# Performance work log

Measured on AMD Instinct MI355X. Metric: run time of the kernel, lower is better.

The kernel has to match this reference:

```python
import jax, jax.numpy as jnp
import numpy as np
import math

D = 256      # d_model
HEADS = 8
PTS = 4      # num_points
L = 6        # num_layers
FF = 1024    # dim_feedforward
B = 8
HS, WS = 100, 100  # feature map -> N = 10000
HD = D // HEADS


def setup_inputs() -> dict:
    key = jax.random.key(0)
    ks = jax.random.split(key, 8)
    w = lambda k, shape, s: jax.random.normal(k, shape, jnp.float32) * s
    z = lambda *shape: jnp.zeros(shape, jnp.float32)
    return {
        "src": jax.random.normal(ks[0], (B, HS * WS, D), jnp.float32),
        "Wv": w(ks[1], (L, D, D), 0.02), "bv": z(L, D),
        "Woff": w(ks[2], (L, D, HEADS * PTS * 2), 0.01), "boff": z(L, HEADS * PTS * 2),
        "Wa": w(ks[3], (L, D, HEADS * PTS), 0.02), "ba": z(L, HEADS * PTS),
        "Wo": w(ks[4], (L, D, D), 0.02), "bo": z(L, D),
        "W1": w(ks[5], (L, D, FF), 0.02), "b1": z(L, FF),
        "W2": w(ks[6], (L, FF, D), 0.02), "b2": z(L, D),
        "g1": jnp.ones((L, D)), "be1": z(L, D),
        "g2": jnp.ones((L, D)), "be2": z(L, D),
        "H": HS, "W": WS,
    }


def pos_encoding_2d(d_model, H, W):
    # standard 2D sine encoding: first half of channels encode y, second half x
    half = d_model // 2
    freqs = jnp.exp(-math.log(10000.0) * jnp.arange(0, half, 2, dtype=jnp.float32) / half)
    ya = jnp.arange(H, dtype=jnp.float32)[:, None] * freqs[None, :]
    xa = jnp.arange(W, dtype=jnp.float32)[:, None] * freqs[None, :]
    pe_y = jnp.stack([jnp.sin(ya), jnp.cos(ya)], -1).reshape(H, half)
    pe_x = jnp.stack([jnp.sin(xa), jnp.cos(xa)], -1).reshape(W, half)
    pe = jnp.concatenate([
        jnp.broadcast_to(pe_y[:, None, :], (H, W, half)),
        jnp.broadcast_to(pe_x[None, :, :], (H, W, half))], -1)
    return pe.reshape(H * W, d_model)


def layer_norm(x, g, b, eps=1e-5):
    m = x.mean(-1, keepdims=True)
    v = ((x - m) ** 2).mean(-1, keepdims=True)
    return (x - m) * jax.lax.rsqrt(v + eps) * g + b


def deform_attn(q, Wv, bv, Woff, boff, Wa, ba, Wo, bo, H, W):
    # single-scale Deformable-DETR attention; q: [B, N, D], N = H*W
    Bq, N, _ = q.shape
    v = (q @ Wv + bv).reshape(Bq, N, HEADS, HD)
    off = (q @ Woff + boff).reshape(Bq, N, HEADS, PTS, 2)          # (dx, dy) in pixels
    attn = jax.nn.softmax((q @ Wa + ba).reshape(Bq, N, HEADS, PTS), axis=-1)
    # reference points: normalized grid cell centers
    ys, xs = jnp.meshgrid(jnp.arange(H, dtype=jnp.float32),
                          jnp.arange(W, dtype=jnp.float32), indexing='ij')
    ref = jnp.stack([(xs.reshape(-1) + 0.5) / W, (ys.reshape(-1) + 0.5) / H], -1)  # [N,2]
    loc = ref[None, :, None, None, :] + off / jnp.array([W, H], jnp.float32)       # [B,N,h,P,2]
    # pixel coords, align_corners=False; border padding via clamping
    px = loc[..., 0] * W - 0.5
    py = loc[..., 1] * H - 0.5
    x0 = jnp.floor(px); y0 = jnp.floor(py)
    wx = px - x0; wy = py - y0
    x0i = jnp.clip(x0.astype(jnp.int32), 0, W - 1); x1i = jnp.clip(x0i + 1, 0, W - 1)
    y0i = jnp.clip(y0.astype(jnp.int32), 0, H - 1); y1i = jnp.clip(y0i + 1, 0, H - 1)
    vbh = v.transpose(0, 2, 1, 3).reshape(Bq * HEADS, N, HD)       # [B*h, N, hd]
    flat = lambda yi, xi: (yi * W + xi).transpose(0, 2, 1, 3).reshape(Bq * HEADS, N * PTS)
    gather = jax.vmap(lambda val, idx: val[idx])                   # [B*h, N*P, hd]
    wxr = wx.transpose(0, 2, 1, 3).reshape(Bq * HEADS, N * PTS, 1)
    wyr = wy.transpose(0, 2, 1, 3).reshape(Bq * HEADS, N * PTS, 1)
    s = (gather(vbh, flat(y0i, x0i)) * (1 - wxr) * (1 - wyr)
         + gather(vbh, flat(y0i, x1i)) * wxr * (1 - wyr)
         + gather(vbh, flat(y1i, x0i)) * (1 - wxr) * wyr
         + gather(vbh, flat(y1i, x1i)) * wxr * wyr)
    s = s.reshape(Bq, HEADS, N, PTS, HD)
    out = jnp.einsum('bhnp,bhnpd->bhnd', attn.transpose(0, 2, 1, 3), s)
    out = out.transpose(0, 2, 1, 3).reshape(Bq, N, D)
    return out @ Wo + bo


def reference(src, Wv, bv, Woff, boff, Wa, ba, Wo, bo, W1, b1, W2, b2,
              g1, be1, g2, be2, H, W):
    x = src + pos_encoding_2d(D, H, W)[None]
    for i in range(L):
        a = deform_attn(x, Wv[i], bv[i], Woff[i], boff[i], Wa[i], ba[i], Wo[i], bo[i], H, W)
        x = layer_norm(x + a, g1[i], be1[i])
        h = jax.nn.gelu(x @ W1[i] + b1[i], approximate=False)
        x = layer_norm(x + (h @ W2[i] + b2[i]), g2[i], be2[i])
    return x
```

## Files before the change

### kernel.cpp

```cpp
#include <hip/hip_runtime.h>
#include <hip/hip_bf16.h>
#include <math.h>

#define Bq   8
#define NPix 10000
#define HH   100
#define WW   100
#define Dm   256
#define NH   8
#define HD   32
#define PTS  4
#define FFd  1024
#define Lnum 6
#define Mrows (Bq * NPix)

typedef short bf16x8 __attribute__((ext_vector_type(8)));
typedef float f32x4 __attribute__((ext_vector_type(4)));

__device__ __forceinline__ float bf2f(unsigned short u) {
    return __uint_as_float(((unsigned)u) << 16);
}
__device__ __forceinline__ unsigned short f2bf(float f) {
    unsigned x = __float_as_uint(f);
    return (unsigned short)((x + 0x7fffu + ((x >> 16) & 1u)) >> 16);
}
__device__ __forceinline__ float gelu_t(float v) {
    float z = 1.5957691216f * (v + 0.044715f * v * v * v);
    float e = __expf(z);
    float th = 1.0f - 2.0f / (e + 1.0f);
    return 0.5f * v * (1.0f + th);
}

__global__ __launch_bounds__(256) void pos_add_kernel(
    const float* __restrict__ src, float* __restrict__ x, short* __restrict__ xb)
{
    int idx = blockIdx.x * 256 + threadIdx.x;
    int c = idx & (Dm - 1);
    int n = (idx >> 8) % NPix;
    int cc = c;
    float coord;
    if (c < 128) { coord = (float)(n / WW); }
    else         { coord = (float)(n % WW); cc = c - 128; }
    int j = cc >> 1;
    float f = __expf(-logf(10000.0f) * (2.0f * (float)j) / 128.0f);
    float arg = coord * f;
    float pe = (cc & 1) ? cosf(arg) : sinf(arg);
    float val = src[idx] + pe;
    x[idx] = val;
    xb[idx] = (short)f2bf(val);
}

__global__ __launch_bounds__(256) void repack_kernel(
    const float* __restrict__ W, short* __restrict__ Wt,
    int K, int N, int outLstride, int nOff)
{
    __shared__ float t[64][65];
    int l  = blockIdx.z;
    int k0 = blockIdx.y * 64, n0 = blockIdx.x * 64;
    const float* Wl = W + (size_t)l * K * N;
    for (int i = threadIdx.x; i < 64 * 64; i += 256) {
        int kk = i >> 6, nn = i & 63;
        float val = 0.0f;
        if (k0 + kk < K && n0 + nn < N) val = Wl[(size_t)(k0 + kk) * N + (n0 + nn)];
        t[kk][nn] = val;
    }
    __syncthreads();
    for (int i = threadIdx.x; i < 64 * 64; i += 256) {
        int nn = i >> 6, kk = i & 63;
        if (n0 + nn < N && k0 + kk < K)
            Wt[(size_t)l * outLstride + (size_t)(nOff + n0 + nn) * K + (k0 + kk)]
                = (short)f2bf(t[kk][nn]);
    }
}

__global__ void bcat_kernel(const float* __restrict__ bv,
                            const float* __restrict__ boff,
                            const float* __restrict__ ba,
                            float* __restrict__ bcat)
{
    int l = blockIdx.x, c = threadIdx.x;
    float v;
    if (c < 256)      v = bv[l * 256 + c];
    else if (c < 320) v = boff[l * 64 + (c - 256)];
    else              v = ba[l * 32 + (c - 320)];
    bcat[l * 352 + c] = v;
}

template<int KI, int MODE>
__global__ __launch_bounds__(256) void gemm_mfma_kernel(
    const short* __restrict__ A, const short* __restrict__ Bt,
    const float* __restrict__ bias, short* __restrict__ Cv,
    float* __restrict__ C2,
    int M, int Nc, int ldc)
{
    constexpr int K = KI * 64;
    __shared__ short As[128 * 64];
    __shared__ short Bs[128 * 64];
    const int tid = threadIdx.x;

    int nwg  = gridDim.x * gridDim.y;
    int orig = blockIdx.y * gridDim.x + blockIdx.x;
    int xcd  = orig & 7, pos = orig >> 3;
    int q = nwg >> 3, r = nwg & 7;
    int flat = (xcd < r ? xcd * (q + 1) : r * (q + 1) + (xcd - r) * q) + pos;
    const int bm = (flat / gridDim.x) * 128;
    const int bn = (flat % gridDim.x) * 128;

    const int w = tid >> 6, l = tid & 63;
    const int wr = (w >> 1) * 64, wc = (w & 1) * 64;
    const int rl = tid >> 3;
    const int cl = tid & 7;
    const int lr = l & 15, lq = l >> 4;

    const short* pA[4]; const short* pB[4];
    #pragma unroll
    for (int p = 0; p < 4; ++p) {
        int row = p * 32 + rl;
        int sc  = cl ^ (row & 7);
        int ga  = bm + row; if (ga > M - 1) ga = M - 1;
        pA[p] = A + (size_t)ga * K + sc * 8;
        int gb  = bn + row; if (gb > Nc - 1) gb = Nc - 1;
        pB[p] = Bt + (size_t)gb * K + sc * 8;
    }

    int aoff[2][4], boff[2][4];
    #pragma unroll
    for (int ks = 0; ks < 2; ++ks)
        #pragma unroll
        for (int m = 0; m < 4; ++m) {
            int ra = wr + m * 16 + lr;
            aoff[ks][m] = ra * 64 + (((ks * 4 + lq) ^ (ra & 7))) * 8;
            int rb = wc + m * 16 + lr;
            boff[ks][m] = rb * 64 + (((ks * 4 + lq) ^ (rb & 7))) * 8;
        }

    f32x4 acc[4][4];
    #pragma unroll
    for (int m = 0; m < 4; ++m)
        #pragma unroll
        for (int n = 0; n < 4; ++n)
            #pragma unroll
            for (int j = 0; j < 4; ++j) acc[m][n][j] = 0.0f;

    #pragma unroll
    for (int kc = 0; kc < KI; ++kc) {
        #pragma unroll
        for (int p = 0; p < 4; ++p) {
            __builtin_amdgcn_global_load_lds((const void*)pA[p],
                (void*)&As[(p * 32 + w * 8) * 64], 16, 0, 0);
            pA[p] += 64;
            __builtin_amdgcn_global_load_lds((const void*)pB[p],
                (void*)&Bs[(p * 32 + w * 8) * 64], 16, 0, 0);
            pB[p] += 64;
        }
        __syncthreads();

        #pragma unroll
        for (int ks = 0; ks < 2; ++ks) {
            bf16x8 af[4], bfr[4];
            #pragma unroll
            for (int m = 0; m < 4; ++m) af[m]  = *(const bf16x8*)&As[aoff[ks][m]];
            #pragma unroll
            for (int n = 0; n < 4; ++n) bfr[n] = *(const bf16x8*)&Bs[boff[ks][n]];
            #pragma unroll
            for (int m = 0; m < 4; ++m)
                #pragma unroll
                for (int n = 0; n < 4; ++n)
                    acc[m][n] = __builtin_amdgcn_mfma_f32_16x16x32_bf16(
                        af[m], bfr[n], acc[m][n], 0, 0, 0);
        }
        __syncthreads();
    }

    #pragma unroll
    for (int m = 0; m < 4; ++m) {
        int row0 = bm + wr + m * 16 + lq * 4;
        #pragma unroll
        for (int n = 0; n < 4; ++n) {
            int col = bn + wc + n * 16 + lr;
            if (MODE == 2 && col >= Nc) continue;
            float bi = bias[col];
            #pragma unroll
            for (int j = 0; j < 4; ++j) {
                int rr = row0 + j;
                if (rr >= M) continue;
                float val = acc[m][n][j] + bi;
                if (MODE == 0) {
                    Cv[(size_t)rr * ldc + col] = (short)f2bf(gelu_t(val));
                } else {
                    if (col < 256)
                        Cv[(size_t)rr * 256 + col] = (short)f2bf(val);
                    else
                        C2[(size_t)rr * 96 + (col - 256)] = val;
                }
            }
        }
    }
}

template<int KI>
__global__ __launch_bounds__(256) void gemm_ln_kernel(
    const short* __restrict__ A, const short* __restrict__ Bt,
    const float* __restrict__ bias,
    const float* __restrict__ gw, const float* __restrict__ bw,
    float* __restrict__ x, short* __restrict__ xb,
    int M)
{
    constexpr int K = KI * 64;
    __shared__ short As[64 * 64];
    __shared__ short Bs[256 * 64];
    const int tid = threadIdx.x;
    const int bm = blockIdx.x * 64;
    const int w = tid >> 6, l = tid & 63;
    const int rl = tid >> 3, cl = tid & 7;
    const int lr = l & 15, lq = l >> 4;

    const short* pA[2]; const short* pB[8];
    #pragma unroll
    for (int p = 0; p < 2; ++p) {
        int row = p * 32 + rl;
        int sc  = cl ^ (row & 7);
        int ga  = bm + row; if (ga > M - 1) ga = M - 1;
        pA[p] = A + (size_t)ga * K + sc * 8;
    }
    #pragma unroll
    for (int p = 0; p < 8; ++p) {
        int row = p * 32 + rl;
        int sc  = cl ^ (row & 7);
        pB[p] = Bt + (size_t)row * K + sc * 8;
    }

    const int arow = w * 16 + lr;
    int aoff[2];
    #pragma unroll
    for (int ks = 0; ks < 2; ++ks)
        aoff[ks] = arow * 64 + (((ks * 4 + lq) ^ (arow & 7))) * 8;
    int boff[2][16];
    #pragma unroll
    for (int ks = 0; ks < 2; ++ks)
        #pragma unroll
        for (int i = 0; i < 16; ++i) {
            int brow = i * 16 + lr;
            boff[ks][i] = brow * 64 + (((ks * 4 + lq) ^ (brow & 7))) * 8;
        }

    f32x4 acc[16];
    #pragma unroll
    for (int n = 0; n < 16; ++n)
        #pragma unroll
        for (int j = 0; j < 4; ++j) acc[n][j] = 0.0f;

    #pragma unroll
    for (int kc = 0; kc < KI; ++kc) {
        #pragma unroll
        for (int p = 0; p < 2; ++p) {
            __builtin_amdgcn_global_load_lds((const void*)pA[p],
                (void*)&As[(p * 32 + w * 8) * 64], 16, 0, 0);
            pA[p] += 64;
        }
        #pragma unroll
        for (int p = 0; p < 8; ++p) {
            __builtin_amdgcn_global_load_lds((const void*)pB[p],
                (void*)&Bs[(p * 32 + w * 8) * 64], 16, 0, 0);
            pB[p] += 64;
        }
        __syncthreads();

        #pragma unroll
        for (int ks = 0; ks < 2; ++ks) {
            bf16x8 af = *(const bf16x8*)&As[aoff[ks]];
            #pragma unroll
            for (int hb = 0; hb < 2; ++hb) {
                bf16x8 bfr[8];
                #pragma unroll
                for (int i = 0; i < 8; ++i)
                    bfr[i] = *(const bf16x8*)&Bs[boff[ks][hb * 8 + i]];
                #pragma unroll
                for (int i = 0; i < 8; ++i)
                    acc[hb * 8 + i] = __builtin_amdgcn_mfma_f32_16x16x32_bf16(
                        af, bfr[i], acc[hb * 8 + i], 0, 0, 0);
            }
        }
        __syncthreads();
    }

    float bi[16];
    #pragma unroll
    for (int n = 0; n < 16; ++n) bi[n] = bias[n * 16 + lr];

    #pragma unroll
    for (int j = 0; j < 4; ++j) {
        int rr = bm + w * 16 + lq * 4 + j;
        if (rr < M) {
            float tmp[16];
            float sum = 0.0f;
            #pragma unroll
            for (int n = 0; n < 16; ++n) {
                int c = n * 16 + lr;
                float val = acc[n][j] + bi[n] + x[(size_t)rr * 256 + c];
                tmp[n] = val;
                sum += val;
            }
            #pragma unroll
            for (int o = 8; o >= 1; o >>= 1) sum += __shfl_xor(sum, o);
            float mean = sum * (1.0f / 256.0f);
            float vs = 0.0f;
            #pragma unroll
            for (int n = 0; n < 16; ++n) {
                float d = tmp[n] - mean;
                vs += d * d;
            }
            #pragma unroll
            for (int o = 8; o >= 1; o >>= 1) vs += __shfl_xor(vs, o);
            float rstd = rsqrtf(vs * (1.0f / 256.0f) + 1e-5f);
            #pragma unroll
            for (int n = 0; n < 16; ++n) {
                int c = n * 16 + lr;
                float ov = (tmp[n] - mean) * rstd * gw[c] + bw[c];
                x[(size_t)rr * 256 + c] = ov;
                xb[(size_t)rr * 256 + c] = (short)f2bf(ov);
            }
        }
    }
}

__global__ __launch_bounds__(256) void deform_attn_kernel(
    const short* __restrict__ v, const float* __restrict__ comb,
    short* __restrict__ outs)
{
    int g  = blockIdx.x * 16 + (threadIdx.x >> 4);
    int d2 = threadIdx.x & 15;
    int bn = g >> 3, h = g & 7;
    int n  = bn % NPix;
    int row = n / WW, col = n % WW;
    int base_v = (bn / NPix) * NPix;

    const float* cb = comb + (size_t)bn * 96;
    float l0 = cb[64 + h * 4 + 0], l1 = cb[64 + h * 4 + 1];
    float l2 = cb[64 + h * 4 + 2], l3 = cb[64 + h * 4 + 3];
    float mx = fmaxf(fmaxf(l0, l1), fmaxf(l2, l3));
    float e0 = __expf(l0 - mx), e1 = __expf(l1 - mx);
    float e2 = __expf(l2 - mx), e3 = __expf(l3 - mx);
    float inv = 1.0f / (e0 + e1 + e2 + e3);
    float aw[4] = {e0 * inv, e1 * inv, e2 * inv, e3 * inv};

    float acc0 = 0.0f, acc1 = 0.0f;
    size_t chb = (size_t)h * HD + d2 * 2;
    #pragma unroll
    for (int p = 0; p < 4; ++p) {
        float dx = cb[h * 8 + p * 2 + 0];
        float dy = cb[h * 8 + p * 2 + 1];
        float px = (float)col + dx;
        float py = (float)row + dy;
        float x0f = floorf(px), y0f = floorf(py);
        float wx = px - x0f, wy = py - y0f;
        int x0i = min(max((int)x0f, 0), WW - 1);
        int y0i = min(max((int)y0f, 0), HH - 1);
        int x1i = min(x0i + 1, WW - 1);
        int y1i = min(y0i + 1, HH - 1);
        unsigned u00 = *(const unsigned*)&v[(size_t)(base_v + y0i * WW + x0i) * Dm + chb];
        unsigned u01 = *(const unsigned*)&v[(size_t)(base_v + y0i * WW + x1i) * Dm + chb];
        unsigned u10 = *(const unsigned*)&v[(size_t)(base_v + y1i * WW + x0i) * Dm + chb];
        unsigned u11 = *(const unsigned*)&v[(size_t)(base_v + y1i * WW + x1i) * Dm + chb];
        float w00 = (1.0f - wx) * (1.0f - wy), w01 = wx * (1.0f - wy);
        float w10 = (1.0f - wx) * wy,          w11 = wx * wy;
        float s0 = bf2f((unsigned short)u00) * w00 + bf2f((unsigned short)u01) * w01
                 + bf2f((unsigned short)u10) * w10 + bf2f((unsigned short)u11) * w11;
        float s1 = bf2f((unsigned short)(u00 >> 16)) * w00 + bf2f((unsigned short)(u01 >> 16)) * w01
                 + bf2f((unsigned short)(u10 >> 16)) * w10 + bf2f((unsigned short)(u11 >> 16)) * w11;
        acc0 = fmaf(aw[p], s0, acc0);
        acc1 = fmaf(aw[p], s1, acc1);
    }
    unsigned outw = (unsigned)f2bf(acc0) | ((unsigned)f2bf(acc1) << 16);
    *(unsigned*)&outs[(size_t)bn * Dm + chb] = outw;
}

extern "C" void kernel_launch(void* const* d_in, const int* in_sizes, int n_in,
                              void* d_out, int out_size, void* d_ws, size_t ws_size,
                              hipStream_t stream)
{
    const float* src  = (const float*)d_in[0];
    const float* Wv   = (const float*)d_in[1];
    const float* bv   = (const float*)d_in[2];
    const float* Woff = (const float*)d_in[3];
    const float* boff = (const float*)d_in[4];
    const float* Wa   = (const float*)d_in[5];
    const float* ba   = (const float*)d_in[6];
    const float* Wo   = (const float*)d_in[7];
    const float* bo   = (const float*)d_in[8];
    const float* W1   = (const float*)d_in[9];
    const float* b1   = (const float*)d_in[10];
    const float* W2   = (const float*)d_in[11];
    const float* b2   = (const float*)d_in[12];
    const float* g1   = (const float*)d_in[13];
    const float* be1  = (const float*)d_in[14];
    const float* g2   = (const float*)d_in[15];
    const float* be2  = (const float*)d_in[16];

    float* x = (float*)d_out;

    char* cur = (char*)d_ws;
    auto take = [&](size_t bytes) { char* p = cur; cur += (bytes + 255) & ~(size_t)255; return p; };
    short* WcatT = (short*)take((size_t)Lnum * 352 * Dm * 2);
    short* WoT   = (short*)take((size_t)Lnum * Dm * Dm * 2);
    short* W1T   = (short*)take((size_t)Lnum * Dm * FFd * 2);
    short* W2T   = (short*)take((size_t)Lnum * FFd * Dm * 2);
    float* bcat  = (float*)take((size_t)Lnum * 352 * 4);
    short* xb    = (short*)take((size_t)Mrows * Dm * 2);
    size_t fixedB = (size_t)(cur - (char*)d_ws);

    const size_t perRowB = 512 + 512 + 384 + 2048;
    int k = 8;
    while (k > 1 && fixedB + (size_t)k * NPix * perRowB > ws_size) k >>= 1;
    if (fixedB + (size_t)k * NPix * perRowB > ws_size) return;
    const int CM = k * NPix;
    const int nChunks = Bq / k;

    short* v    = (short*)take((size_t)CM * Dm * 2);
    short* sbuf = (short*)take((size_t)CM * Dm * 2);
    float* comb = (float*)take((size_t)CM * 96 * 4);
    short* h    = (short*)take((size_t)CM * FFd * 2);

    repack_kernel<<<dim3(4, 4, Lnum),  256, 0, stream>>>(Wv,   WcatT, Dm,  Dm,  352 * Dm,   0);
    repack_kernel<<<dim3(1, 4, Lnum),  256, 0, stream>>>(Woff, WcatT, Dm,  64,  352 * Dm, 256);
    repack_kernel<<<dim3(1, 4, Lnum),  256, 0, stream>>>(Wa,   WcatT, Dm,  32,  352 * Dm, 320);
    repack_kernel<<<dim3(4, 4, Lnum),  256, 0, stream>>>(Wo,   WoT,   Dm,  Dm,  Dm * Dm,    0);
    repack_kernel<<<dim3(16, 4, Lnum), 256, 0, stream>>>(W1,   W1T,   Dm,  FFd, Dm * FFd,   0);
    repack_kernel<<<dim3(4, 16, Lnum), 256, 0, stream>>>(W2,   W2T,   FFd, Dm,  FFd * Dm,   0);
    bcat_kernel<<<Lnum, 352, 0, stream>>>(bv, boff, ba, bcat);

    pos_add_kernel<<<Mrows, 256, 0, stream>>>(src, x, xb);

    const int gy128 = (CM + 127) / 128;
    const int gLN   = (CM + 63) / 64;

    for (int l = 0; l < Lnum; ++l) {
        const short* WcatT_l = WcatT + (size_t)l * 352 * Dm;
        const short* WoT_l   = WoT   + (size_t)l * Dm * Dm;
        const short* W1T_l   = W1T   + (size_t)l * Dm * FFd;
        const short* W2T_l   = W2T   + (size_t)l * FFd * Dm;

        for (int c = 0; c < nChunks; ++c) {
            size_t rowOff = (size_t)c * CM;
            float* xc  = x  + rowOff * Dm;
            short* xbc = xb + rowOff * Dm;

            gemm_mfma_kernel<4, 2><<<dim3(3, gy128), 256, 0, stream>>>(
                xbc, WcatT_l, bcat + l * 352, v, comb, CM, 352, 0);
            deform_attn_kernel<<<CM / 2, 256, 0, stream>>>(v, comb, sbuf);
            gemm_ln_kernel<4><<<gLN, 256, 0, stream>>>(
                sbuf, WoT_l, bo + l * Dm, g1 + l * Dm, be1 + l * Dm, xc, xbc, CM);
            gemm_mfma_kernel<4, 0><<<dim3(8, gy128), 256, 0, stream>>>(
                xbc, W1T_l, b1 + l * FFd, h, nullptr, CM, FFd, FFd);
            gemm_ln_kernel<16><<<gLN, 256, 0, stream>>>(
                h, W2T_l, b2 + l * Dm, g2 + l * Dm, be2 + l * Dm, xc, xbc, CM);
        }
    }
}
```

Baseline: 2.639 ms.

## Double-buffer LDS tiles in GEMM kernels to overlap loads with MFMA

Both the generic MFMA GEMM and the GEMM+LayerNorm kernel now use two LDS buffers. The next K-chunk is issued via global_load_lds before computing on the current one, so global-to-LDS latency overlaps with MFMA work. This doubles LDS usage per block (64KB and 80KB), which may lower occupancy. The loop keeps one syncthreads per iteration, so whether the async LDS writes are correctly ordered against reads of the other buffer is uncertain.

Measured after the change: 2.971 ms. 12.6% more time.

```diff
diff --git a/kernel.cpp b/kernel.cpp
--- a/kernel.cpp
+++ b/kernel.cpp
@@ -94,8 +94,8 @@
     int M, int Nc, int ldc)
 {
     constexpr int K = KI * 64;
-    __shared__ short As[128 * 64];
-    __shared__ short Bs[128 * 64];
+    __shared__ short As[2][128 * 64];
+    __shared__ short Bs[2][128 * 64];
     const int tid = threadIdx.x;
 
     int nwg  = gridDim.x * gridDim.y;
@@ -134,34 +134,41 @@
             boff[ks][m] = rb * 64 + (((ks * 4 + lq) ^ (rb & 7))) * 8;
         }
 
-    f32x4 acc[4][4];
-    #pragma unroll
-    for (int m = 0; m < 4; ++m)
-        #pragma unroll
-        for (int n = 0; n < 4; ++n)
-            #pragma unroll
-            for (int j = 0; j < 4; ++j) acc[m][n][j] = 0.0f;
-
-    #pragma unroll
-    for (int kc = 0; kc < KI; ++kc) {
+    auto stage = [&](int buf) {
         #pragma unroll
         for (int p = 0; p < 4; ++p) {
             __builtin_amdgcn_global_load_lds((const void*)pA[p],
-                (void*)&As[(p * 32 + w * 8) * 64], 16, 0, 0);
+                (void*)&As[buf][(p * 32 + w * 8) * 64], 16, 0, 0);
             pA[p] += 64;
             __builtin_amdgcn_global_load_lds((const void*)pB[p],
-                (void*)&Bs[(p * 32 + w * 8) * 64], 16, 0, 0);
+                (void*)&Bs[buf][(p * 32 + w * 8) * 64], 16, 0, 0);
             pB[p] += 64;
         }
-        __syncthreads();
+    };
+
+    f32x4 acc[4][4];
+    #pragma unroll
+    for (int m = 0; m < 4; ++m)
+        #pragma unroll
+        for (int n = 0; n < 4; ++n)
+            #pragma unroll
+            for (int j = 0; j < 4; ++j) acc[m][n][j] = 0.0f;
+
+    stage(0);
+    __syncthreads();
+
+    #pragma unroll
+    for (int kc = 0; kc < KI; ++kc) {
+        if (kc + 1 < KI) stage((kc + 1) & 1);
+        const int cur = kc & 1;
 
         #pragma unroll
         for (int ks = 0; ks < 2; ++ks) {
             bf16x8 af[4], bfr[4];
             #pragma unroll
-            for (int m = 0; m < 4; ++m) af[m]  = *(const bf16x8*)&As[aoff[ks][m]];
-            #pragma unroll
-            for (int n = 0; n < 4; ++n) bfr[n] = *(const bf16x8*)&Bs[boff[ks][n]];
+            for (int m = 0; m < 4; ++m) af[m]  = *(const bf16x8*)&As[cur][aoff[ks][m]];
+            #pragma unroll
+            for (int n = 0; n < 4; ++n) bfr[n] = *(const bf16x8*)&Bs[cur][boff[ks][n]];
             #pragma unroll
             for (int m = 0; m < 4; ++m)
                 #pragma unroll
@@ -207,8 +214,8 @@
     int M)
 {
     constexpr int K = KI * 64;
-    __shared__ short As[64 * 64];
-    __shared__ short Bs[256 * 64];
+    __shared__ short As[2][64 * 64];
+    __shared__ short Bs[2][256 * 64];
     const int tid = threadIdx.x;
     const int bm = blockIdx.x * 64;
     const int w = tid >> 6, l = tid & 63;
@@ -244,37 +251,44 @@
             boff[ks][i] = brow * 64 + (((ks * 4 + lq) ^ (brow & 7))) * 8;
         }
 
-    f32x4 acc[16];
-    #pragma unroll
-    for (int n = 0; n < 16; ++n)
-        #pragma unroll
-        for (int j = 0; j < 4; ++j) acc[n][j] = 0.0f;
-
-    #pragma unroll
-    for (int kc = 0; kc < KI; ++kc) {
+    auto stage = [&](int buf) {
         #pragma unroll
         for (int p = 0; p < 2; ++p) {
             __builtin_amdgcn_global_load_lds((const void*)pA[p],
-                (void*)&As[(p * 32 + w * 8) * 64], 16, 0, 0);
+                (void*)&As[buf][(p * 32 + w * 8) * 64], 16, 0, 0);
             pA[p] += 64;
         }
         #pragma unroll
         for (int p = 0; p < 8; ++p) {
             __builtin_amdgcn_global_load_lds((const void*)pB[p],
-                (void*)&Bs[(p * 32 + w * 8) * 64], 16, 0, 0);
+                (void*)&Bs[buf][(p * 32 + w * 8) * 64], 16, 0, 0);
             pB[p] += 64;
         }
-        __syncthreads();
+    };
+
+    f32x4 acc[16];
+    #pragma unroll
+    for (int n = 0; n < 16; ++n)
+        #pragma unroll
+        for (int j = 0; j < 4; ++j) acc[n][j] = 0.0f;
+
+    stage(0);
+    __syncthreads();
+
+    #pragma unroll
+    for (int kc = 0; kc < KI; ++kc) {
+        if (kc + 1 < KI) stage((kc + 1) & 1);
+        const int cur = kc & 1;
 
         #pragma unroll
         for (int ks = 0; ks < 2; ++ks) {
-            bf16x8 af = *(const bf16x8*)&As[aoff[ks]];
+            bf16x8 af = *(const bf16x8*)&As[cur][aoff[ks]];
             #pragma unroll
             for (int hb = 0; hb < 2; ++hb) {
                 bf16x8 bfr[8];
                 #pragma unroll
                 for (int i = 0; i < 8; ++i)
-                    bfr[i] = *(const bf16x8*)&Bs[boff[ks][hb * 8 + i]];
+                    bfr[i] = *(const bf16x8*)&Bs[cur][boff[ks][hb * 8 + i]];
                 #pragma unroll
                 for (int i = 0; i < 8; ++i)
                     acc[hb * 8 + i] = __builtin_amdgcn_mfma_f32_16x16x32_bf16(
```
